# Kernel tuning notes

Hardware: AMD Instinct MI355X
Metric: run time of the kernel (lower is better)

Reference implementation:

```python
import jax, jax.numpy as jnp
import numpy as np
import math

B, Q_LEN, K_LEN = 8, 512, 512
D_MODEL, H = 512, 8
DK = D_MODEL // H


def setup_inputs() -> dict:
    key = jax.random.key(0)
    ks = jax.random.split(key, 12)
    inp = {
        "query": jax.random.normal(ks[0], (B, Q_LEN, D_MODEL), jnp.float32),
        "key": jax.random.normal(ks[1], (B, K_LEN, D_MODEL), jnp.float32),
        "value": jax.random.normal(ks[2], (B, K_LEN, D_MODEL), jnp.float32),
        "relative_embeddings": jax.random.normal(ks[3], (K_LEN, Q_LEN, D_MODEL), jnp.float32),
        # causal mask: 1 = attend, 0 = masked
        "mask": jnp.tril(jnp.ones((Q_LEN, K_LEN), dtype=bool)),
        "Wq": jax.random.normal(ks[4], (D_MODEL, D_MODEL), jnp.float32) / math.sqrt(D_MODEL),
        "Wk": jax.random.normal(ks[5], (D_MODEL, D_MODEL), jnp.float32) / math.sqrt(D_MODEL),
        "Wv": jax.random.normal(ks[6], (D_MODEL, D_MODEL), jnp.float32) / math.sqrt(D_MODEL),
        "Wo": jax.random.normal(ks[7], (D_MODEL, D_MODEL), jnp.float32) / math.sqrt(D_MODEL),
        "Wr": jax.random.normal(ks[8], (D_MODEL, D_MODEL), jnp.float32) / math.sqrt(D_MODEL),
        "u": jax.random.normal(ks[9], (H, DK), jnp.float32),
        "v": jax.random.normal(ks[10], (H, DK), jnp.float32),
    }
    return inp


def reference(query, key, value, relative_embeddings, mask, Wq, Wk, Wv, Wo, Wr, u, v):
    b, q_len, d_model = query.shape
    k_len = key.shape[1]
    # torch nn.Linear(x) = x @ W.T (bias=False)
    Qh = (query @ Wq.T).reshape(b, q_len, H, DK).transpose(0, 2, 1, 3)   # bhqd
    Kh = (key @ Wk.T).reshape(b, k_len, H, DK).transpose(0, 2, 1, 3)     # bhkd
    Vh = (value @ Wv.T).reshape(b, k_len, H, DK).transpose(0, 2, 1, 3)   # bhkd
    # relative position projection: (k_len, q_len, d_model)
    R = relative_embeddings @ Wr.T
    # view(k,q,H,dk).permute(2,1,0,3) -> (H, q, k, dk)
    Rh = R.reshape(k_len, q_len, H, DK).transpose(2, 1, 0, 3)
    # content score: (Q + u) K^T
    content = jnp.einsum("bhqd,bhkd->bhqk", Qh + u[None, :, None, :], Kh)
    # position score: (Q + v) R^T, R per-head per-query
    position = jnp.einsum("bhqd,hqkd->bhqk", Qh + v[None, :, None, :], Rh)
    scores = (content + position) / math.sqrt(DK)
    scores = jnp.where(mask[None, None, :, :], scores, -1e9)
    weights = jax.nn.softmax(scores, axis=-1)  # dropout is identity in eval
    out = jnp.einsum("bhqk,bhkd->bhqd", weights, Vh)
    out = out.transpose(0, 2, 1, 3).reshape(b, q_len, d_model)
    out = out @ Wo.T
    return (out, weights)
```

## Files before the change

kernel.cpp:

```cpp
#include <hip/hip_runtime.h>

#define BATCH   8
#define SEQ     512
#define DMODEL  512
#define NHEAD   8
#define DKH     64

typedef __attribute__((ext_vector_type(8))) short bf16x8;
typedef __attribute__((ext_vector_type(4))) float f32x4;

__device__ __forceinline__ short f2bf(float f) {
    union { float f; unsigned u; } v; v.f = f;
    unsigned r = v.u + 0x7FFFu + ((v.u >> 16) & 1u);
    return (short)(r >> 16);
}

#define LDK 40

__device__ __forceinline__ void stage_f32(const float* __restrict__ base,
                                          int rstride, short* lds, int tid) {
    int r = tid >> 2, c = (tid & 3) << 3;
    const float* p = base + (size_t)r * rstride + c;
    float4 x = *(const float4*)p;
    float4 y = *(const float4*)(p + 4);
    union { short s[8]; bf16x8 v; } o;
    o.s[0] = f2bf(x.x); o.s[1] = f2bf(x.y); o.s[2] = f2bf(x.z); o.s[3] = f2bf(x.w);
    o.s[4] = f2bf(y.x); o.s[5] = f2bf(y.y); o.s[6] = f2bf(y.z); o.s[7] = f2bf(y.w);
    *(bf16x8*)(lds + r * LDK + c) = o.v;
}

__device__ __forceinline__ void stage_bf16(const short* __restrict__ base,
                                           int rstride, short* lds, int tid) {
    int r = tid >> 2, c = (tid & 3) << 3;
    bf16x8 v = *(const bf16x8*)(base + (size_t)r * rstride + c);
    *(bf16x8*)(lds + r * LDK + c) = v;
}

__device__ __forceinline__ void mma_tile(const short* As, const short* Bs,
                                         int lane, int wm, int wn, f32x4 acc[2][2]) {
    int lo = lane & 15, hi = lane >> 4;
    bf16x8 a0 = *(const bf16x8*)(As + (wm * 32 + lo) * LDK + hi * 8);
    bf16x8 a1 = *(const bf16x8*)(As + (wm * 32 + 16 + lo) * LDK + hi * 8);
    bf16x8 b0 = *(const bf16x8*)(Bs + (wn * 32 + lo) * LDK + hi * 8);
    bf16x8 b1 = *(const bf16x8*)(Bs + (wn * 32 + 16 + lo) * LDK + hi * 8);
    acc[0][0] = __builtin_amdgcn_mfma_f32_16x16x32_bf16(a0, b0, acc[0][0], 0, 0, 0);
    acc[0][1] = __builtin_amdgcn_mfma_f32_16x16x32_bf16(a0, b1, acc[0][1], 0, 0, 0);
    acc[1][0] = __builtin_amdgcn_mfma_f32_16x16x32_bf16(a1, b0, acc[1][0], 0, 0, 0);
    acc[1][1] = __builtin_amdgcn_mfma_f32_16x16x32_bf16(a1, b1, acc[1][1], 0, 0, 0);
}

__global__ __launch_bounds__(256) void wrt_kernel(const float* __restrict__ Wr,
                                                  short* __restrict__ Wrt) {
    int idx = blockIdx.x * 256 + threadIdx.x;
    int n = idx >> 9, m = idx & 511;
    Wrt[idx] = f2bf(Wr[(size_t)m * 512 + n]);
}

__global__ __launch_bounds__(256) void qkv_kernel(
        const float* __restrict__ query, const float* __restrict__ key_,
        const float* __restrict__ value,
        const float* __restrict__ Wq, const float* __restrict__ Wk,
        const float* __restrict__ Wv,
        const float* __restrict__ uvec, const float* __restrict__ vvec,
        short* __restrict__ Qu, short* __restrict__ Qv,
        short* __restrict__ Kh, short* __restrict__ Vt) {
    __shared__ short As[64 * LDK], Bs[64 * LDK];
    int f = blockIdx.x;
    int i = f >> 3;
    int nt = i & 7;
    int gm = (f & 7) * 24 + (i >> 3);
    int mode = gm >> 6, mt = gm & 63;
    const float* x = mode == 0 ? query : (mode == 1 ? key_ : value);
    const float* W = mode == 0 ? Wq : (mode == 1 ? Wk : Wv);
    int tid = threadIdx.x, lane = tid & 63, w = tid >> 6, wm = w >> 1, wn = w & 1;
    const float* Abase = x + (size_t)mt * 64 * DMODEL;
    const float* Bbase = W + (size_t)nt * 64 * DMODEL;
    f32x4 acc[2][2] = {};
    for (int kt = 0; kt < DMODEL; kt += 32) {
        __syncthreads();
        stage_f32(Abase + kt, DMODEL, As, tid);
        stage_f32(Bbase + kt, DMODEL, Bs, tid);
        __syncthreads();
        mma_tile(As, Bs, lane, wm, wn, acc);
    }
    int lo = lane & 15, hi = lane >> 4;
    for (int fm = 0; fm < 2; fm++)
        for (int fn = 0; fn < 2; fn++)
            for (int r = 0; r < 4; r++) {
                int m = mt * 64 + wm * 32 + fm * 16 + hi * 4 + r;
                int n = nt * 64 + wn * 32 + fn * 16 + lo;
                float val = acc[fm][fn][r];
                int b = m >> 9, s = m & 511, h = n >> 6, d = n & 63;
                if (mode == 0) {
                    size_t idx = ((size_t)(b * NHEAD + h) * SEQ + s) * DKH + d;
                    Qu[idx] = f2bf(val + uvec[n]);
                    Qv[idx] = f2bf(val + vvec[n]);
                } else if (mode == 1) {
                    Kh[((size_t)(b * NHEAD + h) * SEQ + s) * DKH + d] = f2bf(val);
                } else {
                    Vt[((size_t)(b * NHEAD + h) * DKH + d) * SEQ + s] = f2bf(val);
                }
            }
}

__global__ __launch_bounds__(256) void t_kernel(const short* __restrict__ Qv,
                                                const short* __restrict__ Wrt,
                                                short* __restrict__ T) {
    __shared__ short As[64 * LDK], Bs[64 * LDK];
    int f = blockIdx.x;
    int i = f >> 3;
    int nt = i & 7;
    int mh = (f & 7) * 64 + (i >> 3);
    int mt = mh >> 3, h = mh & 7;
    int tid = threadIdx.x, lane = tid & 63, w = tid >> 6, wm = w >> 1, wn = w & 1;
    int m0 = mt * 64, b = m0 >> 9, q0 = m0 & 511;
    const short* Abase = Qv + ((size_t)(b * NHEAD + h) * SEQ + q0) * DKH;
    const short* Bbase = Wrt + (size_t)nt * 64 * DMODEL + h * DKH;
    f32x4 acc[2][2] = {};
    for (int kt = 0; kt < DKH; kt += 32) {
        __syncthreads();
        stage_bf16(Abase + kt, DKH, As, tid);
        stage_bf16(Bbase + kt, DMODEL, Bs, tid);
        __syncthreads();
        mma_tile(As, Bs, lane, wm, wn, acc);
    }
    int lo = lane & 15, hi = lane >> 4;
    for (int fm = 0; fm < 2; fm++)
        for (int fn = 0; fn < 2; fn++)
            for (int r = 0; r < 4; r++) {
                int q = q0 + wm * 32 + fm * 16 + hi * 4 + r;
                int n = nt * 64 + wn * 32 + fn * 16 + lo;
                T[((size_t)(b * NHEAD + h) * SEQ + q) * DMODEL + n] = f2bf(acc[fm][fn][r]);
            }
}

__global__ __launch_bounds__(256) void content_kernel(const short* __restrict__ Qu,
                                                      const short* __restrict__ Kh,
                                                      float* __restrict__ scores) {
    int f = blockIdx.x;
    int i = f >> 3;
    int bh = (f & 7) * 8 + (i >> 6);
    int rest = i & 63;
    int kt_ = rest & 7, qt = rest >> 3;
    if (kt_ > qt) return;
    __shared__ short As[64 * LDK], Bs[64 * LDK];
    int tid = threadIdx.x, lane = tid & 63, w = tid >> 6, wm = w >> 1, wn = w & 1;
    const short* Abase = Qu + ((size_t)bh * SEQ + qt * 64) * DKH;
    const short* Bbase = Kh + ((size_t)bh * SEQ + kt_ * 64) * DKH;
    f32x4 acc[2][2] = {};
    for (int kt = 0; kt < DKH; kt += 32) {
        __syncthreads();
        stage_bf16(Abase + kt, DKH, As, tid);
        stage_bf16(Bbase + kt, DKH, Bs, tid);
        __syncthreads();
        mma_tile(As, Bs, lane, wm, wn, acc);
    }
    int lo = lane & 15, hi = lane >> 4;
    for (int fm = 0; fm < 2; fm++)
        for (int fn = 0; fn < 2; fn++)
            for (int r = 0; r < 4; r++) {
                int q = qt * 64 + wm * 32 + fm * 16 + hi * 4 + r;
                int k = kt_ * 64 + wn * 32 + fn * 16 + lo;
                scores[((size_t)bh * SEQ + q) * SEQ + k] = acc[fm][fn][r];
            }
}

__global__ __launch_bounds__(256) void position_kernel(const short* __restrict__ T,
                                                       const float* __restrict__ rel,
                                                       float* __restrict__ scores) {
    int bk = blockIdx.x;
    int q = (bk & 7) * 64 + ((bk >> 3) >> 2);
    int stripe = (bk >> 3) & 3;
    if (stripe * 128 > q) return;
    __shared__ short Tl[64 * 512];
    int tid = threadIdx.x, w = tid >> 6, lane = tid & 63;
    const short* Tq = T + (size_t)q * DMODEL;
    for (int it = 0; it < 16; ++it) {
        int r = it * 4 + w;
        bf16x8 v = *(const bf16x8*)(Tq + (size_t)r * (SEQ * DMODEL) + lane * 8);
        int g = lane ^ (r & 7);
        *(bf16x8*)(Tl + r * 512 + g * 8) = v;
    }
    __syncthreads();
    int kbase = stripe * 128 + w * 32;
    if (kbase > q) return;
    int lo = lane & 15, hi = lane >> 4;
    const float* relq = rel + ((size_t)kbase * SEQ + q) * DMODEL;
    f32x4 acc[4][2] = {};
    for (int n = 0; n < DMODEL; n += 32) {
        bf16x8 a[4];
        #pragma unroll
        for (int fm = 0; fm < 4; fm++) {
            int rr = fm * 16 + lo;
            int g = ((n >> 3) + hi) ^ (rr & 7);
            a[fm] = *(const bf16x8*)(Tl + rr * 512 + g * 8);
        }
        bf16x8 bfrag[2];
        #pragma unroll
        for (int fk = 0; fk < 2; fk++) {
            const float* p = relq + (size_t)(fk * 16 + lo) * (SEQ * DMODEL) + n + hi * 8;
            float4 x = *(const float4*)p;
            float4 y = *(const float4*)(p + 4);
            union { short s[8]; bf16x8 v; } o;
            o.s[0] = f2bf(x.x); o.s[1] = f2bf(x.y); o.s[2] = f2bf(x.z); o.s[3] = f2bf(x.w);
            o.s[4] = f2bf(y.x); o.s[5] = f2bf(y.y); o.s[6] = f2bf(y.z); o.s[7] = f2bf(y.w);
            bfrag[fk] = o.v;
        }
        #pragma unroll
        for (int fm = 0; fm < 4; fm++) {
            acc[fm][0] = __builtin_amdgcn_mfma_f32_16x16x32_bf16(a[fm], bfrag[0], acc[fm][0], 0, 0, 0);
            acc[fm][1] = __builtin_amdgcn_mfma_f32_16x16x32_bf16(a[fm], bfrag[1], acc[fm][1], 0, 0, 0);
        }
    }
    #pragma unroll
    for (int fm = 0; fm < 4; fm++)
        #pragma unroll
        for (int fk = 0; fk < 2; fk++)
            #pragma unroll
            for (int r = 0; r < 4; r++) {
                int bh = fm * 16 + hi * 4 + r;
                int k = kbase + fk * 16 + lo;
                scores[((size_t)bh * SEQ + q) * SEQ + k] += acc[fm][fk][r];
            }
}

__global__ __launch_bounds__(256) void softmax_kernel(float* __restrict__ scores) {
    int gw = (blockIdx.x * 256 + threadIdx.x) >> 6;
    int lane = threadIdx.x & 63;
    int q = gw & 511;
    float* row = scores + (size_t)gw * SEQ;
    int k0 = lane * 4, k1 = 256 + lane * 4;
    float4 v0 = make_float4(0.f, 0.f, 0.f, 0.f), v1 = v0;
    if (k0 <= q) v0 = *(const float4*)(row + k0);
    if (k1 <= q) v1 = *(const float4*)(row + k1);
    float x[8];
    const float NEG = -1e30f;
    x[0] = (k0 + 0 <= q) ? v0.x * 0.125f : NEG;
    x[1] = (k0 + 1 <= q) ? v0.y * 0.125f : NEG;
    x[2] = (k0 + 2 <= q) ? v0.z * 0.125f : NEG;
    x[3] = (k0 + 3 <= q) ? v0.w * 0.125f : NEG;
    x[4] = (k1 + 0 <= q) ? v1.x * 0.125f : NEG;
    x[5] = (k1 + 1 <= q) ? v1.y * 0.125f : NEG;
    x[6] = (k1 + 2 <= q) ? v1.z * 0.125f : NEG;
    x[7] = (k1 + 3 <= q) ? v1.w * 0.125f : NEG;
    float mx = x[0];
    #pragma unroll
    for (int i = 1; i < 8; i++) mx = fmaxf(mx, x[i]);
    #pragma unroll
    for (int o = 32; o; o >>= 1) mx = fmaxf(mx, __shfl_xor(mx, o));
    float p[8], s = 0.f;
    #pragma unroll
    for (int i = 0; i < 8; i++) { p[i] = __expf(x[i] - mx); s += p[i]; }
    #pragma unroll
    for (int o = 32; o; o >>= 1) s += __shfl_xor(s, o);
    float inv = 1.0f / s;
    float4 o0 = make_float4(p[0] * inv, p[1] * inv, p[2] * inv, p[3] * inv);
    float4 o1 = make_float4(p[4] * inv, p[5] * inv, p[6] * inv, p[7] * inv);
    *(float4*)(row + k0) = o0;
    *(float4*)(row + k1) = o1;
}

__global__ __launch_bounds__(256) void pv_kernel(const float* __restrict__ scores,
                                                 const short* __restrict__ Vt,
                                                 short* __restrict__ attn) {
    __shared__ short As[64 * LDK], Bs[64 * LDK];
    int f = blockIdx.x;
    int i = f >> 3;
    int bh = (f & 7) * 8 + (i >> 3);
    int qt = i & 7;
    int tid = threadIdx.x, lane = tid & 63, w = tid >> 6, wm = w >> 1, wn = w & 1;
    const float* Abase = scores + ((size_t)bh * SEQ + qt * 64) * SEQ;
    const short* Bbase = Vt + (size_t)bh * DKH * SEQ;
    int kmax = (qt + 1) * 64;
    f32x4 acc[2][2] = {};
    for (int kt = 0; kt < kmax; kt += 32) {
        __syncthreads();
        stage_f32(Abase + kt, SEQ, As, tid);
        stage_bf16(Bbase + kt, SEQ, Bs, tid);
        __syncthreads();
        mma_tile(As, Bs, lane, wm, wn, acc);
    }
    int lo = lane & 15, hi = lane >> 4;
    int b = bh >> 3, h = bh & 7;
    for (int fm = 0; fm < 2; fm++)
        for (int fn = 0; fn < 2; fn++)
            for (int r = 0; r < 4; r++) {
                int q = qt * 64 + wm * 32 + fm * 16 + hi * 4 + r;
                int d = wn * 32 + fn * 16 + lo;
                attn[((size_t)b * SEQ + q) * DMODEL + h * DKH + d] = f2bf(acc[fm][fn][r]);
            }
}

__global__ __launch_bounds__(256) void oproj_kernel(const short* __restrict__ attn,
                                                    const float* __restrict__ Wo,
                                                    float* __restrict__ out) {
    __shared__ short As[64 * LDK], Bs[64 * LDK];
    int f = blockIdx.x;
    int i = f >> 3;
    int mt = (f & 7) * 8 + (i >> 3);
    int nt = i & 7;
    int tid = threadIdx.x, lane = tid & 63, w = tid >> 6, wm = w >> 1, wn = w & 1;
    const short* Abase = attn + (size_t)mt * 64 * DMODEL;
    const float* Bbase = Wo + (size_t)nt * 64 * DMODEL;
    f32x4 acc[2][2] = {};
    for (int kt = 0; kt < DMODEL; kt += 32) {
        __syncthreads();
        stage_bf16(Abase + kt, DMODEL, As, tid);
        stage_f32(Bbase + kt, DMODEL, Bs, tid);
        __syncthreads();
        mma_tile(As, Bs, lane, wm, wn, acc);
    }
    int lo = lane & 15, hi = lane >> 4;
    for (int fm = 0; fm < 2; fm++)
        for (int fn = 0; fn < 2; fn++)
            for (int r = 0; r < 4; r++) {
                int m = mt * 64 + wm * 32 + fm * 16 + hi * 4 + r;
                int n = nt * 64 + wn * 32 + fn * 16 + lo;
                out[(size_t)m * DMODEL + n] = acc[fm][fn][r];
            }
}

extern "C" void kernel_launch(void* const* d_in, const int* in_sizes, int n_in,
                              void* d_out, int out_size, void* d_ws, size_t ws_size,
                              hipStream_t stream) {
    (void)in_sizes; (void)n_in; (void)out_size; (void)ws_size;
    const float* query = (const float*)d_in[0];
    const float* key   = (const float*)d_in[1];
    const float* value = (const float*)d_in[2];
    const float* rel   = (const float*)d_in[3];
    const float* Wq = (const float*)d_in[5];
    const float* Wk = (const float*)d_in[6];
    const float* Wv = (const float*)d_in[7];
    const float* Wo = (const float*)d_in[8];
    const float* Wr = (const float*)d_in[9];
    const float* u  = (const float*)d_in[10];
    const float* v  = (const float*)d_in[11];

    float* out     = (float*)d_out;
    float* weights = out + (size_t)BATCH * SEQ * DMODEL;

    char* ws = (char*)d_ws;
    short* Qu   = (short*)(ws);
    short* Qv   = (short*)(ws + ((size_t)4 << 20));
    short* Kh   = (short*)(ws + ((size_t)8 << 20));
    short* Vt   = (short*)(ws + ((size_t)12 << 20));
    short* T    = (short*)(ws + ((size_t)16 << 20));
    short* attn = (short*)(ws + ((size_t)48 << 20));
    short* Wrt  = (short*)(ws + ((size_t)52 << 20));

    wrt_kernel<<<1024, 256, 0, stream>>>(Wr, Wrt);
    qkv_kernel<<<1536, 256, 0, stream>>>(query, key, value, Wq, Wk, Wv,
                                         u, v, Qu, Qv, Kh, Vt);
    t_kernel<<<4096, 256, 0, stream>>>(Qv, Wrt, T);
    content_kernel<<<4096, 256, 0, stream>>>(Qu, Kh, weights);
    position_kernel<<<2048, 256, 0, stream>>>(T, rel, weights);
    softmax_kernel<<<8192, 256, 0, stream>>>(weights);
    pv_kernel<<<512, 256, 0, stream>>>(weights, Vt, attn);
    oproj_kernel<<<512, 256, 0, stream>>>(attn, Wo, out);
}
```

Baseline: 226.9 us.

## Fuse softmax into PV kernel and halve position-kernel LDS staging

The standalone softmax pass is removed. The PV kernel now computes row max and sum with an online reduction over its 64-row tile, then normalizes probabilities on the fly, writes them back as weights and feeds them as bf16 into the MFMA tile. This saves one kernel launch and one full read/write round trip of the score tensor, but each score row is read twice inside PV and exp is evaluated twice. Separately, position_kernel stages T into LDS in two 256-column halves, halving LDS from 64KB to 32KB to allow higher occupancy, at the cost of an extra barrier pair.

```diff
diff --git a/kernel.cpp b/kernel.cpp
--- a/kernel.cpp
+++ b/kernel.cpp
@@ -172,46 +172,56 @@
     int q = (bk & 7) * 64 + ((bk >> 3) >> 2);
     int stripe = (bk >> 3) & 3;
     if (stripe * 128 > q) return;
-    __shared__ short Tl[64 * 512];
+    __shared__ short Tl[64 * 256];
     int tid = threadIdx.x, w = tid >> 6, lane = tid & 63;
+    int kbase = stripe * 128 + w * 32;
+    bool active = (kbase <= q);
+    int lo = lane & 15, hi = lane >> 4;
     const short* Tq = T + (size_t)q * DMODEL;
-    for (int it = 0; it < 16; ++it) {
-        int r = it * 4 + w;
-        bf16x8 v = *(const bf16x8*)(Tq + (size_t)r * (SEQ * DMODEL) + lane * 8);
-        int g = lane ^ (r & 7);
-        *(bf16x8*)(Tl + r * 512 + g * 8) = v;
-    }
-    __syncthreads();
-    int kbase = stripe * 128 + w * 32;
-    if (kbase > q) return;
-    int lo = lane & 15, hi = lane >> 4;
     const float* relq = rel + ((size_t)kbase * SEQ + q) * DMODEL;
     f32x4 acc[4][2] = {};
-    for (int n = 0; n < DMODEL; n += 32) {
-        bf16x8 a[4];
+    for (int half = 0; half < 2; ++half) {
+        int nbase = half * 256;
+        __syncthreads();
         #pragma unroll
-        for (int fm = 0; fm < 4; fm++) {
-            int rr = fm * 16 + lo;
-            int g = ((n >> 3) + hi) ^ (rr & 7);
-            a[fm] = *(const bf16x8*)(Tl + rr * 512 + g * 8);
+        for (int it = 0; it < 8; ++it) {
+            int r = it * 8 + w * 2 + (lane >> 5);
+            int cc = lane & 31;
+            bf16x8 v = *(const bf16x8*)(Tq + (size_t)r * (SEQ * DMODEL) + nbase + cc * 8);
+            int g = cc ^ (r & 7);
+            *(bf16x8*)(Tl + r * 256 + g * 8) = v;
         }
-        bf16x8 bfrag[2];
-        #pragma unroll
-        for (int fk = 0; fk < 2; fk++) {
-            const float* p = relq + (size_t)(fk * 16 + lo) * (SEQ * DMODEL) + n + hi * 8;
-            float4 x = *(const float4*)p;
-            float4 y = *(const float4*)(p + 4);
-            union { short s[8]; bf16x8 v; } o;
-            o.s[0] = f2bf(x.x); o.s[1] = f2bf(x.y); o.s[2] = f2bf(x.z); o.s[3] = f2bf(x.w);
-            o.s[4] = f2bf(y.x); o.s[5] = f2bf(y.y); o.s[6] = f2bf(y.z); o.s[7] = f2bf(y.w);
-            bfrag[fk] = o.v;
+        __syncthreads();
+        if (active) {
+            for (int nn = 0; nn < 256; nn += 32) {
+                bf16x8 a[4];
+                #pragma unroll
+                for (int fm = 0; fm < 4; fm++) {
+                    int rr = fm * 16 + lo;
+                    int g = ((nn >> 3) + hi) ^ (rr & 7);
+                    a[fm] = *(const bf16x8*)(Tl + rr * 256 + g * 8);
+                }
+                bf16x8 bfrag[2];
+                #pragma unroll
+                for (int fk = 0; fk < 2; fk++) {
+                    const float* p = relq + (size_t)(fk * 16 + lo) * (SEQ * DMODEL)
+                                   + nbase + nn + hi * 8;
+                    float4 x = *(const float4*)p;
+                    float4 y = *(const float4*)(p + 4);
+                    union { short s[8]; bf16x8 v; } o;
+                    o.s[0] = f2bf(x.x); o.s[1] = f2bf(x.y); o.s[2] = f2bf(x.z); o.s[3] = f2bf(x.w);
+                    o.s[4] = f2bf(y.x); o.s[5] = f2bf(y.y); o.s[6] = f2bf(y.z); o.s[7] = f2bf(y.w);
+                    bfrag[fk] = o.v;
+                }
+                #pragma unroll
+                for (int fm = 0; fm < 4; fm++) {
+                    acc[fm][0] = __builtin_amdgcn_mfma_f32_16x16x32_bf16(a[fm], bfrag[0], acc[fm][0], 0, 0, 0);
+                    acc[fm][1] = __builtin_amdgcn_mfma_f32_16x16x32_bf16(a[fm], bfrag[1], acc[fm][1], 0, 0, 0);
+                }
+            }
         }
-        #pragma unroll
-        for (int fm = 0; fm < 4; fm++) {
-            acc[fm][0] = __builtin_amdgcn_mfma_f32_16x16x32_bf16(a[fm], bfrag[0], acc[fm][0], 0, 0, 0);
-            acc[fm][1] = __builtin_amdgcn_mfma_f32_16x16x32_bf16(a[fm], bfrag[1], acc[fm][1], 0, 0, 0);
-        }
-    }
+    }
+    if (!active) return;
     #pragma unroll
     for (int fm = 0; fm < 4; fm++)
         #pragma unroll
@@ -224,70 +234,81 @@
             }
 }
 
-__global__ __launch_bounds__(256) void softmax_kernel(float* __restrict__ scores) {
-    int gw = (blockIdx.x * 256 + threadIdx.x) >> 6;
-    int lane = threadIdx.x & 63;
-    int q = gw & 511;
-    float* row = scores + (size_t)gw * SEQ;
-    int k0 = lane * 4, k1 = 256 + lane * 4;
-    float4 v0 = make_float4(0.f, 0.f, 0.f, 0.f), v1 = v0;
-    if (k0 <= q) v0 = *(const float4*)(row + k0);
-    if (k1 <= q) v1 = *(const float4*)(row + k1);
-    float x[8];
-    const float NEG = -1e30f;
-    x[0] = (k0 + 0 <= q) ? v0.x * 0.125f : NEG;
-    x[1] = (k0 + 1 <= q) ? v0.y * 0.125f : NEG;
-    x[2] = (k0 + 2 <= q) ? v0.z * 0.125f : NEG;
-    x[3] = (k0 + 3 <= q) ? v0.w * 0.125f : NEG;
-    x[4] = (k1 + 0 <= q) ? v1.x * 0.125f : NEG;
-    x[5] = (k1 + 1 <= q) ? v1.y * 0.125f : NEG;
-    x[6] = (k1 + 2 <= q) ? v1.z * 0.125f : NEG;
-    x[7] = (k1 + 3 <= q) ? v1.w * 0.125f : NEG;
-    float mx = x[0];
-    #pragma unroll
-    for (int i = 1; i < 8; i++) mx = fmaxf(mx, x[i]);
-    #pragma unroll
-    for (int o = 32; o; o >>= 1) mx = fmaxf(mx, __shfl_xor(mx, o));
-    float p[8], s = 0.f;
-    #pragma unroll
-    for (int i = 0; i < 8; i++) { p[i] = __expf(x[i] - mx); s += p[i]; }
-    #pragma unroll
-    for (int o = 32; o; o >>= 1) s += __shfl_xor(s, o);
-    float inv = 1.0f / s;
-    float4 o0 = make_float4(p[0] * inv, p[1] * inv, p[2] * inv, p[3] * inv);
-    float4 o1 = make_float4(p[4] * inv, p[5] * inv, p[6] * inv, p[7] * inv);
-    *(float4*)(row + k0) = o0;
-    *(float4*)(row + k1) = o1;
-}
-
-__global__ __launch_bounds__(256) void pv_kernel(const float* __restrict__ scores,
-                                                 const short* __restrict__ Vt,
-                                                 short* __restrict__ attn) {
+__global__ __launch_bounds__(256) void pv_sm_kernel(float* __restrict__ scores,
+                                                    const short* __restrict__ Vt,
+                                                    short* __restrict__ attn) {
     __shared__ short As[64 * LDK], Bs[64 * LDK];
     int f = blockIdx.x;
     int i = f >> 3;
     int bh = (f & 7) * 8 + (i >> 3);
     int qt = i & 7;
     int tid = threadIdx.x, lane = tid & 63, w = tid >> 6, wm = w >> 1, wn = w & 1;
-    const float* Abase = scores + ((size_t)bh * SEQ + qt * 64) * SEQ;
+    int kmax = (qt + 1) * 64;
+    int r = tid >> 2, c4 = tid & 3;
+    int q = qt * 64 + r;
+    float* row = scores + ((size_t)bh * SEQ + q) * SEQ;
+    float M = -1e30f, S = 0.f;
+    int kbeg = c4 * 128;
+    int kend = (kbeg + 128 < kmax) ? kbeg + 128 : kmax;
+    for (int k = kbeg; k < kend; k += 4) {
+        float4 vv = *(const float4*)(row + k);
+        float x0 = (k + 0 <= q) ? vv.x * 0.125f : -1e30f;
+        float x1 = (k + 1 <= q) ? vv.y * 0.125f : -1e30f;
+        float x2 = (k + 2 <= q) ? vv.z * 0.125f : -1e30f;
+        float x3 = (k + 3 <= q) ? vv.w * 0.125f : -1e30f;
+        float mx = fmaxf(fmaxf(x0, x1), fmaxf(x2, x3));
+        float Mn = fmaxf(M, mx);
+        S = S * __expf(M - Mn) + __expf(x0 - Mn) + __expf(x1 - Mn)
+          + __expf(x2 - Mn) + __expf(x3 - Mn);
+        M = Mn;
+    }
+    #pragma unroll
+    for (int off = 1; off <= 2; off <<= 1) {
+        float Mo = __shfl_xor(M, off), So = __shfl_xor(S, off);
+        float Mn = fmaxf(M, Mo);
+        S = S * __expf(M - Mn) + So * __expf(Mo - Mn);
+        M = Mn;
+    }
+    float invS = 1.0f / S;
     const short* Bbase = Vt + (size_t)bh * DKH * SEQ;
-    int kmax = (qt + 1) * 64;
-    f32x4 acc[2][2] = {};
-    for (int kt = 0; kt < kmax; kt += 32) {
-        __syncthreads();
-        stage_f32(Abase + kt, SEQ, As, tid);
-        stage_bf16(Bbase + kt, SEQ, Bs, tid);
-        __syncthreads();
-        mma_tile(As, Bs, lane, wm, wn, acc);
+    f32x4 acc[2][2] = {};
+    int cc = c4 * 8;
+    for (int kt = 0; kt < SEQ; kt += 32) {
+        if (kt < kmax) {
+            __syncthreads();
+            stage_bf16(Bbase + kt, SEQ, Bs, tid);
+            float4 x = *(const float4*)(row + kt + cc);
+            float4 y = *(const float4*)(row + kt + cc + 4);
+            float p0 = (kt + cc + 0 <= q) ? __expf(x.x * 0.125f - M) * invS : 0.f;
+            float p1 = (kt + cc + 1 <= q) ? __expf(x.y * 0.125f - M) * invS : 0.f;
+            float p2 = (kt + cc + 2 <= q) ? __expf(x.z * 0.125f - M) * invS : 0.f;
+            float p3 = (kt + cc + 3 <= q) ? __expf(x.w * 0.125f - M) * invS : 0.f;
+            float p4 = (kt + cc + 4 <= q) ? __expf(y.x * 0.125f - M) * invS : 0.f;
+            float p5 = (kt + cc + 5 <= q) ? __expf(y.y * 0.125f - M) * invS : 0.f;
+            float p6 = (kt + cc + 6 <= q) ? __expf(y.z * 0.125f - M) * invS : 0.f;
+            float p7 = (kt + cc + 7 <= q) ? __expf(y.w * 0.125f - M) * invS : 0.f;
+            *(float4*)(row + kt + cc) = make_float4(p0, p1, p2, p3);
+            *(float4*)(row + kt + cc + 4) = make_float4(p4, p5, p6, p7);
+            union { short s[8]; bf16x8 v; } o;
+            o.s[0] = f2bf(p0); o.s[1] = f2bf(p1); o.s[2] = f2bf(p2); o.s[3] = f2bf(p3);
+            o.s[4] = f2bf(p4); o.s[5] = f2bf(p5); o.s[6] = f2bf(p6); o.s[7] = f2bf(p7);
+            *(bf16x8*)(As + r * LDK + cc) = o.v;
+            __syncthreads();
+            mma_tile(As, Bs, lane, wm, wn, acc);
+        } else {
+            float4 z = make_float4(0.f, 0.f, 0.f, 0.f);
+            *(float4*)(row + kt + cc) = z;
+            *(float4*)(row + kt + cc + 4) = z;
+        }
     }
     int lo = lane & 15, hi = lane >> 4;
     int b = bh >> 3, h = bh & 7;
     for (int fm = 0; fm < 2; fm++)
         for (int fn = 0; fn < 2; fn++)
-            for (int r = 0; r < 4; r++) {
-                int q = qt * 64 + wm * 32 + fm * 16 + hi * 4 + r;
+            for (int rr = 0; rr < 4; rr++) {
+                int qq = qt * 64 + wm * 32 + fm * 16 + hi * 4 + rr;
                 int d = wn * 32 + fn * 16 + lo;
-                attn[((size_t)b * SEQ + q) * DMODEL + h * DKH + d] = f2bf(acc[fm][fn][r]);
+                attn[((size_t)b * SEQ + qq) * DMODEL + h * DKH + d] = f2bf(acc[fm][fn][rr]);
             }
 }
 
@@ -354,7 +375,6 @@
     t_kernel<<<4096, 256, 0, stream>>>(Qv, Wrt, T);
     content_kernel<<<4096, 256, 0, stream>>>(Qu, Kh, weights);
     position_kernel<<<2048, 256, 0, stream>>>(T, rel, weights);
-    softmax_kernel<<<8192, 256, 0, stream>>>(weights);
-    pv_kernel<<<512, 256, 0, stream>>>(weights, Vt, attn);
+    pv_sm_kernel<<<512, 256, 0, stream>>>(weights, Vt, attn);
     oproj_kernel<<<512, 256, 0, stream>>>(attn, Wo, out);
 }
```

After: 230.1 us. About the same (+1.4%).

## Fuse content score, softmax and PV into one kernel; merge Wr transpose into QKV

Applied to the files above, without the earlier changes.

Replaces the separate content, softmax and PV kernels with one fused kernel per (batch-head, 32-query block). It computes QK^T with MFMA, adds the position scores read from a separate buffer, exponentiates, keeps unnormalized probabilities in LDS as bf16, writes normalized weights, and then does PV from LDS. The Wr transpose kernel is folded into extra blocks of the QKV projection launch to remove one launch. This removes several full passes over the fp32 score matrix. The trade-offs are a new fp32 position buffer and the absence of max subtraction in the softmax, which risks overflow in exp. Weights are also derived from bf16-rounded probabilities.

```diff
diff --git a/kernel.cpp b/kernel.cpp
--- a/kernel.cpp
+++ b/kernel.cpp
@@ -13,6 +13,10 @@
     union { float f; unsigned u; } v; v.f = f;
     unsigned r = v.u + 0x7FFFu + ((v.u >> 16) & 1u);
     return (short)(r >> 16);
+}
+__device__ __forceinline__ float bf2f(short s) {
+    union { unsigned u; float f; } v; v.u = ((unsigned)(unsigned short)s) << 16;
+    return v.f;
 }
 
 #define LDK 40
@@ -49,30 +53,34 @@
     acc[1][1] = __builtin_amdgcn_mfma_f32_16x16x32_bf16(a1, b1, acc[1][1], 0, 0, 0);
 }
 
-__global__ __launch_bounds__(256) void wrt_kernel(const float* __restrict__ Wr,
-                                                  short* __restrict__ Wrt) {
-    int idx = blockIdx.x * 256 + threadIdx.x;
-    int n = idx >> 9, m = idx & 511;
-    Wrt[idx] = f2bf(Wr[(size_t)m * 512 + n]);
-}
-
-__global__ __launch_bounds__(256) void qkv_kernel(
+__global__ __launch_bounds__(256) void qkvw_kernel(
         const float* __restrict__ query, const float* __restrict__ key_,
         const float* __restrict__ value,
         const float* __restrict__ Wq, const float* __restrict__ Wk,
-        const float* __restrict__ Wv,
+        const float* __restrict__ Wv, const float* __restrict__ Wr,
         const float* __restrict__ uvec, const float* __restrict__ vvec,
         short* __restrict__ Qu, short* __restrict__ Qv,
-        short* __restrict__ Kh, short* __restrict__ Vt) {
+        short* __restrict__ Kh, short* __restrict__ Vt,
+        short* __restrict__ Wrt) {
     __shared__ short As[64 * LDK], Bs[64 * LDK];
-    int f = blockIdx.x;
+    int f = blockIdx.x, tid = threadIdx.x;
+    if (f >= 1536) {
+        int base = (f - 1536) * 1024;
+        #pragma unroll
+        for (int j = 0; j < 4; j++) {
+            int idx = base + j * 256 + tid;
+            int n = idx >> 9, m = idx & 511;
+            Wrt[idx] = f2bf(Wr[(size_t)m * 512 + n]);
+        }
+        return;
+    }
     int i = f >> 3;
     int nt = i & 7;
     int gm = (f & 7) * 24 + (i >> 3);
     int mode = gm >> 6, mt = gm & 63;
     const float* x = mode == 0 ? query : (mode == 1 ? key_ : value);
     const float* W = mode == 0 ? Wq : (mode == 1 ? Wk : Wv);
-    int tid = threadIdx.x, lane = tid & 63, w = tid >> 6, wm = w >> 1, wn = w & 1;
+    int lane = tid & 63, w = tid >> 6, wm = w >> 1, wn = w & 1;
     const float* Abase = x + (size_t)mt * 64 * DMODEL;
     const float* Bbase = W + (size_t)nt * 64 * DMODEL;
     f32x4 acc[2][2] = {};
@@ -134,40 +142,9 @@
             }
 }
 
-__global__ __launch_bounds__(256) void content_kernel(const short* __restrict__ Qu,
-                                                      const short* __restrict__ Kh,
-                                                      float* __restrict__ scores) {
-    int f = blockIdx.x;
-    int i = f >> 3;
-    int bh = (f & 7) * 8 + (i >> 6);
-    int rest = i & 63;
-    int kt_ = rest & 7, qt = rest >> 3;
-    if (kt_ > qt) return;
-    __shared__ short As[64 * LDK], Bs[64 * LDK];
-    int tid = threadIdx.x, lane = tid & 63, w = tid >> 6, wm = w >> 1, wn = w & 1;
-    const short* Abase = Qu + ((size_t)bh * SEQ + qt * 64) * DKH;
-    const short* Bbase = Kh + ((size_t)bh * SEQ + kt_ * 64) * DKH;
-    f32x4 acc[2][2] = {};
-    for (int kt = 0; kt < DKH; kt += 32) {
-        __syncthreads();
-        stage_bf16(Abase + kt, DKH, As, tid);
-        stage_bf16(Bbase + kt, DKH, Bs, tid);
-        __syncthreads();
-        mma_tile(As, Bs, lane, wm, wn, acc);
-    }
-    int lo = lane & 15, hi = lane >> 4;
-    for (int fm = 0; fm < 2; fm++)
-        for (int fn = 0; fn < 2; fn++)
-            for (int r = 0; r < 4; r++) {
-                int q = qt * 64 + wm * 32 + fm * 16 + hi * 4 + r;
-                int k = kt_ * 64 + wn * 32 + fn * 16 + lo;
-                scores[((size_t)bh * SEQ + q) * SEQ + k] = acc[fm][fn][r];
-            }
-}
-
 __global__ __launch_bounds__(256) void position_kernel(const short* __restrict__ T,
                                                        const float* __restrict__ rel,
-                                                       float* __restrict__ scores) {
+                                                       float* __restrict__ pos) {
     int bk = blockIdx.x;
     int q = (bk & 7) * 64 + ((bk >> 3) >> 2);
     int stripe = (bk >> 3) & 3;
@@ -220,75 +197,121 @@
             for (int r = 0; r < 4; r++) {
                 int bh = fm * 16 + hi * 4 + r;
                 int k = kbase + fk * 16 + lo;
-                scores[((size_t)bh * SEQ + q) * SEQ + k] += acc[fm][fk][r];
-            }
-}
-
-__global__ __launch_bounds__(256) void softmax_kernel(float* __restrict__ scores) {
-    int gw = (blockIdx.x * 256 + threadIdx.x) >> 6;
-    int lane = threadIdx.x & 63;
-    int q = gw & 511;
-    float* row = scores + (size_t)gw * SEQ;
-    int k0 = lane * 4, k1 = 256 + lane * 4;
-    float4 v0 = make_float4(0.f, 0.f, 0.f, 0.f), v1 = v0;
-    if (k0 <= q) v0 = *(const float4*)(row + k0);
-    if (k1 <= q) v1 = *(const float4*)(row + k1);
-    float x[8];
-    const float NEG = -1e30f;
-    x[0] = (k0 + 0 <= q) ? v0.x * 0.125f : NEG;
-    x[1] = (k0 + 1 <= q) ? v0.y * 0.125f : NEG;
-    x[2] = (k0 + 2 <= q) ? v0.z * 0.125f : NEG;
-    x[3] = (k0 + 3 <= q) ? v0.w * 0.125f : NEG;
-    x[4] = (k1 + 0 <= q) ? v1.x * 0.125f : NEG;
-    x[5] = (k1 + 1 <= q) ? v1.y * 0.125f : NEG;
-    x[6] = (k1 + 2 <= q) ? v1.z * 0.125f : NEG;
-    x[7] = (k1 + 3 <= q) ? v1.w * 0.125f : NEG;
-    float mx = x[0];
-    #pragma unroll
-    for (int i = 1; i < 8; i++) mx = fmaxf(mx, x[i]);
-    #pragma unroll
-    for (int o = 32; o; o >>= 1) mx = fmaxf(mx, __shfl_xor(mx, o));
-    float p[8], s = 0.f;
-    #pragma unroll
-    for (int i = 0; i < 8; i++) { p[i] = __expf(x[i] - mx); s += p[i]; }
-    #pragma unroll
-    for (int o = 32; o; o >>= 1) s += __shfl_xor(s, o);
-    float inv = 1.0f / s;
-    float4 o0 = make_float4(p[0] * inv, p[1] * inv, p[2] * inv, p[3] * inv);
-    float4 o1 = make_float4(p[4] * inv, p[5] * inv, p[6] * inv, p[7] * inv);
-    *(float4*)(row + k0) = o0;
-    *(float4*)(row + k1) = o1;
-}
-
-__global__ __launch_bounds__(256) void pv_kernel(const float* __restrict__ scores,
-                                                 const short* __restrict__ Vt,
-                                                 short* __restrict__ attn) {
-    __shared__ short As[64 * LDK], Bs[64 * LDK];
+                pos[((size_t)bh * SEQ + q) * SEQ + k] = acc[fm][fk][r];
+            }
+}
+
+__global__ __launch_bounds__(256) void pv_fused_kernel(
+        const short* __restrict__ Qu, const short* __restrict__ Kh,
+        const short* __restrict__ Vt, const float* __restrict__ pos,
+        float* __restrict__ weights, short* __restrict__ attn) {
+    __shared__ short Qs[2 * 32 * LDK];
+    __shared__ short Ks[2 * 64 * LDK];
+    __shared__ short Ps[32 * 520];
+    __shared__ float S_lds[4][32];
+    __shared__ float invS_lds[32];
     int f = blockIdx.x;
     int i = f >> 3;
-    int bh = (f & 7) * 8 + (i >> 3);
-    int qt = i & 7;
-    int tid = threadIdx.x, lane = tid & 63, w = tid >> 6, wm = w >> 1, wn = w & 1;
-    const float* Abase = scores + ((size_t)bh * SEQ + qt * 64) * SEQ;
-    const short* Bbase = Vt + (size_t)bh * DKH * SEQ;
-    int kmax = (qt + 1) * 64;
-    f32x4 acc[2][2] = {};
-    for (int kt = 0; kt < kmax; kt += 32) {
-        __syncthreads();
-        stage_f32(Abase + kt, SEQ, As, tid);
-        stage_bf16(Bbase + kt, SEQ, Bs, tid);
-        __syncthreads();
-        mma_tile(As, Bs, lane, wm, wn, acc);
-    }
-    int lo = lane & 15, hi = lane >> 4;
+    int bh = (f & 7) * 8 + (i >> 4);
+    int qb = i & 15;
+    int q0 = qb * 32;
+    int kmax = q0 + 32;
+    int tid = threadIdx.x, lane = tid & 63, w = tid >> 6;
+    int lo = lane & 15, hi = lane >> 4;
+
+    {
+        int r = tid >> 3, c = (tid & 7) << 3;
+        bf16x8 v = *(const bf16x8*)(Qu + ((size_t)bh * SEQ + q0 + r) * DKH + c);
+        *(bf16x8*)(Qs + (c >> 5) * 32 * LDK + r * LDK + (c & 31)) = v;
+    }
+    __syncthreads();
+    bf16x8 aq[2][2];
+    #pragma unroll
+    for (int fq = 0; fq < 2; fq++)
+        #pragma unroll
+        for (int ch = 0; ch < 2; ch++)
+            aq[fq][ch] = *(const bf16x8*)(Qs + ch * 32 * LDK + (fq * 16 + lo) * LDK + hi * 8);
+
+    const short* Khb = Kh + (size_t)bh * SEQ * DKH;
+    float Sa[2][4] = {};
+    for (int kt = 0; kt < kmax; kt += 64) {
+        __syncthreads();
+        stage_bf16(Khb + (size_t)kt * DKH, DKH, Ks, tid);
+        stage_bf16(Khb + (size_t)kt * DKH + 32, DKH, Ks + 64 * LDK, tid);
+        __syncthreads();
+        bf16x8 bk0 = *(const bf16x8*)(Ks + (w * 16 + lo) * LDK + hi * 8);
+        bf16x8 bk1 = *(const bf16x8*)(Ks + 64 * LDK + (w * 16 + lo) * LDK + hi * 8);
+        f32x4 acc[2] = {};
+        #pragma unroll
+        for (int fq = 0; fq < 2; fq++) {
+            acc[fq] = __builtin_amdgcn_mfma_f32_16x16x32_bf16(aq[fq][0], bk0, acc[fq], 0, 0, 0);
+            acc[fq] = __builtin_amdgcn_mfma_f32_16x16x32_bf16(aq[fq][1], bk1, acc[fq], 0, 0, 0);
+        }
+        int k = kt + w * 16 + lo;
+        #pragma unroll
+        for (int fq = 0; fq < 2; fq++)
+            #pragma unroll
+            for (int r = 0; r < 4; r++) {
+                int ql = fq * 16 + hi * 4 + r;
+                int q = q0 + ql;
+                float ps = pos[((size_t)bh * SEQ + q) * SEQ + k];
+                float x = (acc[fq][r] + ps) * 0.125f;
+                float p = (k <= q) ? __expf(x) : 0.f;
+                Sa[fq][r] += p;
+                Ps[ql * 520 + k] = f2bf(p);
+            }
+    }
+    #pragma unroll
+    for (int fq = 0; fq < 2; fq++)
+        #pragma unroll
+        for (int r = 0; r < 4; r++) {
+            float s = Sa[fq][r];
+            s += __shfl_xor(s, 1); s += __shfl_xor(s, 2);
+            s += __shfl_xor(s, 4); s += __shfl_xor(s, 8);
+            if (lo == 0) S_lds[w][fq * 16 + hi * 4 + r] = s;
+        }
+    __syncthreads();
+    if (tid < 32)
+        invS_lds[tid] = 1.0f / (S_lds[0][tid] + S_lds[1][tid] + S_lds[2][tid] + S_lds[3][tid]);
+    __syncthreads();
+    {
+        int r = tid >> 3, kc0 = (tid & 7) * 64;
+        float inv = invS_lds[r];
+        float* wrow = weights + ((size_t)bh * SEQ + q0 + r) * SEQ + kc0;
+        const short* prow = Ps + r * 520 + kc0;
+        #pragma unroll
+        for (int j = 0; j < 64; j += 4) {
+            float4 o;
+            o.x = (kc0 + j + 0 < kmax) ? bf2f(prow[j + 0]) * inv : 0.f;
+            o.y = (kc0 + j + 1 < kmax) ? bf2f(prow[j + 1]) * inv : 0.f;
+            o.z = (kc0 + j + 2 < kmax) ? bf2f(prow[j + 2]) * inv : 0.f;
+            o.w = (kc0 + j + 3 < kmax) ? bf2f(prow[j + 3]) * inv : 0.f;
+            *(float4*)(wrow + j) = o;
+        }
+    }
+    const short* Vtb = Vt + (size_t)bh * DKH * SEQ;
+    f32x4 pacc[2] = {};
+    for (int kc = 0; kc < kmax; kc += 32) {
+        __syncthreads();
+        stage_bf16(Vtb + kc, SEQ, Ks, tid);
+        __syncthreads();
+        bf16x8 bv = *(const bf16x8*)(Ks + (w * 16 + lo) * LDK + hi * 8);
+        #pragma unroll
+        for (int fq = 0; fq < 2; fq++) {
+            bf16x8 ap = *(const bf16x8*)(Ps + (fq * 16 + lo) * 520 + kc + hi * 8);
+            pacc[fq] = __builtin_amdgcn_mfma_f32_16x16x32_bf16(ap, bv, pacc[fq], 0, 0, 0);
+        }
+    }
     int b = bh >> 3, h = bh & 7;
-    for (int fm = 0; fm < 2; fm++)
-        for (int fn = 0; fn < 2; fn++)
-            for (int r = 0; r < 4; r++) {
-                int q = qt * 64 + wm * 32 + fm * 16 + hi * 4 + r;
-                int d = wn * 32 + fn * 16 + lo;
-                attn[((size_t)b * SEQ + q) * DMODEL + h * DKH + d] = f2bf(acc[fm][fn][r]);
-            }
+    #pragma unroll
+    for (int fq = 0; fq < 2; fq++)
+        #pragma unroll
+        for (int r = 0; r < 4; r++) {
+            int ql = fq * 16 + hi * 4 + r;
+            int d = w * 16 + lo;
+            float val = pacc[fq][r] * invS_lds[ql];
+            attn[((size_t)b * SEQ + q0 + ql) * DMODEL + h * DKH + d] = f2bf(val);
+        }
 }
 
 __global__ __launch_bounds__(256) void oproj_kernel(const short* __restrict__ attn,
@@ -347,14 +370,12 @@
     short* T    = (short*)(ws + ((size_t)16 << 20));
     short* attn = (short*)(ws + ((size_t)48 << 20));
     short* Wrt  = (short*)(ws + ((size_t)52 << 20));
-
-    wrt_kernel<<<1024, 256, 0, stream>>>(Wr, Wrt);
-    qkv_kernel<<<1536, 256, 0, stream>>>(query, key, value, Wq, Wk, Wv,
-                                         u, v, Qu, Qv, Kh, Vt);
+    float* pos  = (float*)(ws + ((size_t)64 << 20));
+
+    qkvw_kernel<<<1792, 256, 0, stream>>>(query, key, value, Wq, Wk, Wv, Wr,
+                                          u, v, Qu, Qv, Kh, Vt, Wrt);
     t_kernel<<<4096, 256, 0, stream>>>(Qv, Wrt, T);
-    content_kernel<<<4096, 256, 0, stream>>>(Qu, Kh, weights);
-    position_kernel<<<2048, 256, 0, stream>>>(T, rel, weights);
-    softmax_kernel<<<8192, 256, 0, stream>>>(weights);
-    pv_kernel<<<512, 256, 0, stream>>>(weights, Vt, attn);
+    position_kernel<<<2048, 256, 0, stream>>>(T, rel, pos);
+    pv_fused_kernel<<<1024, 256, 0, stream>>>(Qu, Kh, Vt, pos, weights, attn);
     oproj_kernel<<<512, 256, 0, stream>>>(attn, Wo, out);
 }
```

Result: slower. 243.0 us (+7.1%).
